# Performance work log

Hardware: AMD Instinct MI355X
Metric: run time of the kernel (lower is better)

## Reference

```python
import jax, jax.numpy as jnp
import numpy as np

D = 2048      # d_model
H = 16        # n_heads
DH = D // H   # head dim = 128
L = 512       # kv_latent_dim
B = 2
S = 2048      # new tokens
PAST = 2048   # cached latent positions


def _w(key, shape, fan_in):
    return jax.random.normal(key, shape, jnp.float32) * (fan_in ** -0.5)


def setup_inputs() -> dict:
    key = jax.random.key(0)
    ks = jax.random.split(key, 8)
    return {
        "x": jax.random.normal(ks[0], (B, S, D), jnp.float32),
        "kv_cache": jax.random.normal(ks[1], (B, PAST, L), jnp.float32),
        "W_q": _w(ks[2], (D, D), D),       # nn.Linear weight [out, in]
        "W_dkv": _w(ks[3], (L, D), D),
        "W_uk": _w(ks[4], (D, L), L),
        "W_uv": _w(ks[5], (D, L), L),
        "W_o": _w(ks[6], (D, D), D),
        "ln_g": jnp.ones((L,), jnp.float32),
        "ln_b": jnp.zeros((L,), jnp.float32),
        "past_length": PAST,
    }


def _layernorm(x, g, b, eps=1e-5):
    mu = jnp.mean(x, axis=-1, keepdims=True)
    var = jnp.mean((x - mu) ** 2, axis=-1, keepdims=True)
    return (x - mu) * jax.lax.rsqrt(var + eps) * g + b


def reference(x, kv_cache, W_q, W_dkv, W_uk, W_uv, W_o, ln_g, ln_b, past_length):
    Bx, Sx, _ = x.shape
    # absorbed_k = W_q.weight @ W_uk.weight -> [D, L] -> [H, dh, L]
    absorbed = (W_q @ W_uk).reshape(H, DH, L)
    # compress to latent KV and layernorm
    new_c = _layernorm(x @ W_dkv.T, ln_g, ln_b)          # [B, S, L]
    c_kv = jnp.concatenate([kv_cache, new_c], axis=1)    # [B, T, L]
    T = c_kv.shape[1]
    # decompress V only
    v = (c_kv @ W_uv.T).reshape(Bx, T, H, DH).transpose(0, 2, 1, 3)  # [B, H, T, dh]
    # absorbed Q/K: scores_h = x_h @ absorbed_k[h] @ c_kv^T
    q = x.reshape(Bx, Sx, H, DH)                          # [B, S, H, dh]
    tmp = jnp.einsum('bshd,hdl->bhsl', q, absorbed)       # [B, H, S, L]
    scale = jnp.float32(1.0 / np.sqrt(DH))
    scores = jnp.einsum('bhsl,btl->bhst', tmp, c_kv) * scale  # [B, H, S, T]
    # causal mask: row i attends to cols j with j <= i + past_length
    mask = jnp.tril(jnp.ones((Sx, T), dtype=bool), k=past_length)
    scores = jnp.where(mask, scores, -jnp.inf)
    w = jax.nn.softmax(scores, axis=-1)
    ctx = jnp.einsum('bhst,bhtd->bshd', w, v).reshape(Bx, Sx, D)
    out = ctx @ W_o.T
    return out, c_kv
```

## Files before the change

### kernel.cpp

```cpp
#include <hip/hip_runtime.h>
#include <cstdint>

#define DV 2048
#define HH 16
#define DHD 128
#define LL 512
#define BB 2

typedef __attribute__((ext_vector_type(8))) short bf16x8;
typedef __attribute__((ext_vector_type(4))) float f32x4;
typedef __attribute__((ext_vector_type(4))) int i32x4;

typedef __attribute__((address_space(1))) const void* gas_cp;
typedef __attribute__((address_space(3))) void* las_p;

__device__ __forceinline__ void gll16(const void* g, void* l) {
    __builtin_amdgcn_global_load_lds((gas_cp)g, (las_p)l, 16, 0, 0);
}

__device__ __forceinline__ unsigned short f2b(float f) {
    union { float f; unsigned int u; } v; v.f = f;
    unsigned int u = v.u;
    return (unsigned short)((u + 0x7FFFu + ((u >> 16) & 1u)) >> 16);
}

__device__ __forceinline__ unsigned int cvt_pk_bf16(float lo, float hi) {
    unsigned int r;
    asm("v_cvt_pk_bf16_f32 %0, %1, %2" : "=v"(r) : "v"(lo), "v"(hi));
    return r;
}

#if __has_builtin(__builtin_amdgcn_exp2f)
#define EX2(x) __builtin_amdgcn_exp2f(x)
#else
#define EX2(x) exp2f(x)
#endif

__global__ void cvt_k(const float* __restrict__ in, ushort* __restrict__ out, long n) {
    long stride = (long)gridDim.x * blockDim.x * 4;
    for (long i = ((long)blockIdx.x * blockDim.x + threadIdx.x) * 4; i < n; i += stride) {
        float4 f = *(const float4*)(in + i);
        *(ushort4*)(out + i) = make_ushort4(f2b(f.x), f2b(f.y), f2b(f.z), f2b(f.w));
    }
}

__global__ void transpose_cvt_k(const float* __restrict__ in, ushort* __restrict__ outp,
                                int R, int C) {
    __shared__ float tile[64][65];
    int c0 = blockIdx.x * 64, r0 = blockIdx.y * 64;
    int tx = threadIdx.x & 63, ty = threadIdx.x >> 6;
#pragma unroll
    for (int p = 0; p < 16; ++p)
        tile[ty + p * 4][tx] = in[(long)(r0 + ty + p * 4) * C + c0 + tx];
    __syncthreads();
#pragma unroll
    for (int p = 0; p < 16; ++p)
        outp[(long)(c0 + ty + p * 4) * R + r0 + tx] = f2b(tile[tx][ty + p * 4]);
}

__global__ void kvcopy_k(const float* __restrict__ kv, float* __restrict__ cko,
                         ushort* __restrict__ ckb, int PAST, int T) {
    long n = (long)BB * PAST * LL;
    long pl2 = (long)PAST * LL;
    long stride = (long)gridDim.x * blockDim.x * 4;
    for (long i = ((long)blockIdx.x * blockDim.x + threadIdx.x) * 4; i < n; i += stride) {
        float4 f = *(const float4*)(kv + i);
        long b = i / pl2, wloc = i - b * pl2;
        long o = b * (long)T * LL + wloc;
        *(float4*)(cko + o) = f;
        *(ushort4*)(ckb + o) = make_ushort4(f2b(f.x), f2b(f.y), f2b(f.z), f2b(f.w));
    }
}

__global__ __launch_bounds__(256) void ln_k(const float* __restrict__ cpre,
                                            const float* __restrict__ g, const float* __restrict__ be,
                                            float* __restrict__ cko, ushort* __restrict__ ckb,
                                            int S, int PAST, int T) {
    int wid = threadIdx.x >> 6, lane = threadIdx.x & 63;
    int row = blockIdx.x * 4 + wid;
    int b = row / S, s = row - b * S;
    const float* xr = cpre + (long)row * LL + lane * 8;
    float4 v0 = *(const float4*)xr;
    float4 v1 = *(const float4*)(xr + 4);
    float sum = v0.x + v0.y + v0.z + v0.w + v1.x + v1.y + v1.z + v1.w;
    float sq = v0.x * v0.x + v0.y * v0.y + v0.z * v0.z + v0.w * v0.w +
               v1.x * v1.x + v1.y * v1.y + v1.z * v1.z + v1.w * v1.w;
#pragma unroll
    for (int m = 1; m < 64; m <<= 1) { sum += __shfl_xor(sum, m, 64); sq += __shfl_xor(sq, m, 64); }
    float mu = sum * (1.0f / LL);
    float var = sq * (1.0f / LL) - mu * mu;
    float rstd = rsqrtf(var + 1e-5f);
    const float* gp = g + lane * 8;
    const float* bp = be + lane * 8;
    float4 g0 = *(const float4*)gp, g1 = *(const float4*)(gp + 4);
    float4 b0 = *(const float4*)bp, b1 = *(const float4*)(bp + 4);
    float y0 = (v0.x - mu) * rstd * g0.x + b0.x;
    float y1 = (v0.y - mu) * rstd * g0.y + b0.y;
    float y2 = (v0.z - mu) * rstd * g0.z + b0.z;
    float y3 = (v0.w - mu) * rstd * g0.w + b0.w;
    float y4 = (v1.x - mu) * rstd * g1.x + b1.x;
    float y5 = (v1.y - mu) * rstd * g1.y + b1.y;
    float y6 = (v1.z - mu) * rstd * g1.z + b1.z;
    float y7 = (v1.w - mu) * rstd * g1.w + b1.w;
    long o = ((long)b * T + PAST + s) * LL + lane * 8;
    *(float4*)(cko + o) = make_float4(y0, y1, y2, y3);
    *(float4*)(cko + o + 4) = make_float4(y4, y5, y6, y7);
    *(ushort4*)(ckb + o) = make_ushort4(f2b(y0), f2b(y1), f2b(y2), f2b(y3));
    *(ushort4*)(ckb + o + 4) = make_ushort4(f2b(y4), f2b(y5), f2b(y6), f2b(y7));
}

template <bool OUT_BF16>
__global__ __launch_bounds__(256, 2) void gemm_nt(const ushort* __restrict__ A,
                                                  const ushort* __restrict__ B,
                                                  void* __restrict__ Cv,
                                                  int K, int lda, int ldb, int ldc,
                                                  long aHi, long aLo, long bHi, long bLo,
                                                  long cHi, long cLo, int zdiv, float cscale) {
    __shared__ __align__(16) ushort Asm[128 * 72];
    __shared__ __align__(16) ushort Bsm[128 * 72];
    const int tid = threadIdx.x, wid = tid >> 6, lane = tid & 63;
    const int z = blockIdx.z, zh = z / zdiv, zl = z % zdiv;
    A += zh * aHi + zl * aLo;
    B += zh * bHi + zl * bLo;
    const long cOff = zh * cHi + zl * cLo;
    const int m0 = blockIdx.x * 128, n0 = blockIdx.y * 128;
    const int wm = (wid >> 1) * 64, wn = (wid & 1) * 64;
    f32x4 acc[4][4] = {};
    const int l8 = lane & 7;
    const int rowA = wid * 8 + (lane >> 3);
    const ushort* Ag = A + (long)(m0 + rowA) * lda + l8 * 8;
    const ushort* Bg = B + (long)(n0 + rowA) * ldb + l8 * 8;

    i32x4 ra[4], rb[4];
#pragma unroll
    for (int p = 0; p < 4; ++p) {
        ra[p] = *(const i32x4*)(Ag + (long)p * 32 * lda);
        rb[p] = *(const i32x4*)(Bg + (long)p * 32 * ldb);
    }
    for (int kt = 0; kt < K; kt += 64) {
        __syncthreads();
#pragma unroll
        for (int p = 0; p < 4; ++p) {
            *(i32x4*)(Asm + (p * 32 + rowA) * 72 + l8 * 8) = ra[p];
            *(i32x4*)(Bsm + (p * 32 + rowA) * 72 + l8 * 8) = rb[p];
        }
        __syncthreads();
        if (kt + 64 < K) {
#pragma unroll
            for (int p = 0; p < 4; ++p) {
                ra[p] = *(const i32x4*)(Ag + (long)p * 32 * lda + kt + 64);
                rb[p] = *(const i32x4*)(Bg + (long)p * 32 * ldb + kt + 64);
            }
        }
#pragma unroll
        for (int kk = 0; kk < 2; ++kk) {
            const int ko = kk * 32 + ((lane >> 4) << 3);
            bf16x8 af[4], bf[4];
#pragma unroll
            for (int i = 0; i < 4; ++i)
                af[i] = *(const bf16x8*)(Asm + (wm + i * 16 + (lane & 15)) * 72 + ko);
#pragma unroll
            for (int j = 0; j < 4; ++j)
                bf[j] = *(const bf16x8*)(Bsm + (wn + j * 16 + (lane & 15)) * 72 + ko);
#pragma unroll
            for (int i = 0; i < 4; ++i)
#pragma unroll
                for (int j = 0; j < 4; ++j)
                    acc[i][j] = __builtin_amdgcn_mfma_f32_16x16x32_bf16(af[i], bf[j], acc[i][j], 0, 0, 0);
        }
        __syncthreads();
    }
    const int cr = (lane >> 4) * 4, cc = lane & 15;
#pragma unroll
    for (int i = 0; i < 4; ++i) {
#pragma unroll
        for (int r = 0; r < 4; ++r) {
            const long row = m0 + wm + i * 16 + cr + r;
#pragma unroll
            for (int j = 0; j < 4; ++j) {
                const long col = n0 + wn + j * 16 + cc;
                if (OUT_BF16)
                    ((ushort*)Cv)[cOff + row * ldc + col] = f2b(acc[i][j][r] * cscale);
                else
                    ((float*)Cv)[cOff + row * ldc + col] = acc[i][j][r] * cscale;
            }
        }
    }
}

#define PH_WAIT4()                                               \
    do {                                                         \
        asm volatile("s_waitcnt vmcnt(4) lgkmcnt(0)" ::: "memory"); \
        __builtin_amdgcn_s_barrier();                            \
    } while (0)
#define PH_WAIT0()                                               \
    do {                                                         \
        asm volatile("s_waitcnt vmcnt(0) lgkmcnt(0)" ::: "memory"); \
        __builtin_amdgcn_s_barrier();                            \
    } while (0)
#define RD_BAR()                                                 \
    do {                                                         \
        asm volatile("s_waitcnt lgkmcnt(0)" ::: "memory");       \
        __builtin_amdgcn_s_barrier();                            \
    } while (0)

__global__ __launch_bounds__(256, 4) void attn_k(const ushort* __restrict__ qbf,
                                                 const ushort* __restrict__ ktb,
                                                 const ushort* __restrict__ vtb,
                                                 ushort* __restrict__ ctxb,
                                                 int S, int T, int PAST) {
    __shared__ __align__(16) ushort bufK[64 * 128];
    __shared__ __align__(16) ushort bufV[128 * 64];
    __shared__ __align__(16) ushort pl[4][16][64];
    const int tid = threadIdx.x, wid = tid >> 6, lane = tid & 63;
    const int nsb = S >> 6;
    const int nwg = BB * HH * nsb;
    const int cpx = nwg >> 3;
    const int id = (int)blockIdx.x;
    const int xcd = id & 7, k = id >> 3;
    const int r4 = k >> 5, c32 = k & 31;
    const int local = r4 * 32 + ((c32 + r4 * 8) & 31);
    const int orig = xcd * cpx + local;
    const int sblk = orig % nsb;
    const int h = (orig / nsb) % HH;
    const int b = orig / (nsb * HH);
    const int s0 = (nsb - 1 - sblk) * 64;

    const int g = lane >> 4, l15 = lane & 15, q8 = g << 3;
    const int swr = (l15 & 7) << 3;

    bf16x8 qf[4];
    {
        const ushort* qb = qbf + ((long)b * S + s0 + wid * 16 + l15) * DV + h * DHD + q8;
#pragma unroll
        for (int kk = 0; kk < 4; ++kk) qf[kk] = *(const bf16x8*)(qb + kk * 32);
    }
    f32x4 cacc[8] = {};
    f32x4 sacc[4] = {};
    float mrow = -1e30f, lrow = 0.f;
    const int rl = tid >> 4, cc16 = tid & 15;
    const int vr = tid >> 3, vc = tid & 7;
    const int nfull = (s0 + PAST) / 64;
    const ushort* kbase = ktb + (long)b * T * DV + h * DHD;
    const ushort* vbase = vtb + ((long)b * DV + h * DHD) * T;
    const int kcol = (cc16 ^ (rl & 7)) << 3;
    const int vcol = (vc ^ (vr & 7)) << 3;

    auto stageK = [&](int tt_) {
#pragma unroll
        for (int p = 0; p < 4; ++p)
            gll16(kbase + (long)(tt_ * 64 + p * 16 + rl) * DV + kcol, &bufK[p * 2048 + tid * 8]);
    };
    auto stageV = [&](int tt_) {
#pragma unroll
        for (int p = 0; p < 4; ++p)
            gll16(vbase + (long)(p * 32 + vr) * T + tt_ * 64 + vcol, &bufV[p * 2048 + tid * 8]);
    };

    stageK(0);
    stageV(0);

    for (int tt = 0; tt <= nfull; ++tt) {
        const bool last = (tt == nfull);
        PH_WAIT4();
        __builtin_amdgcn_s_setprio(1);
#pragma unroll
        for (int kk = 0; kk < 4; ++kk) {
            const int ko = kk * 32 + q8;
#pragma unroll
            for (int nf = 0; nf < 4; ++nf) {
                bf16x8 af = *(const bf16x8*)(&bufK[(nf * 16 + l15) * 128 + (ko ^ swr)]);
                sacc[nf] = __builtin_amdgcn_mfma_f32_16x16x32_bf16(af, qf[kk], sacc[nf], 0, 0, 0);
            }
        }
        __builtin_amdgcn_s_setprio(0);
        RD_BAR();
        if (!last) stageK(tt + 1);
        if (last) { PH_WAIT0(); } else { PH_WAIT4(); }
        float pm = -1e30f;
#pragma unroll
        for (int nf = 0; nf < 4; ++nf)
#pragma unroll
            for (int r = 0; r < 4; ++r) {
                float v = sacc[nf][r];
                if (last) {
                    int tl = nf * 16 + (g << 2) + r;
                    int ql = wid * 16 + l15;
                    if (tl > ql) v = -1e30f;
                }
                sacc[nf][r] = v;
                pm = fmaxf(pm, v);
            }
        pm = fmaxf(pm, __shfl_xor(pm, 16, 64));
        pm = fmaxf(pm, __shfl_xor(pm, 32, 64));
        if (__any(pm > mrow + 11.5f)) {
            float mn = fmaxf(mrow, pm);
            float al = EX2(mrow - mn);
            mrow = mn;
            lrow *= al;
#pragma unroll
            for (int r = 0; r < 4; ++r) {
                float alr = __shfl(al, (g << 2) + r, 64);
#pragma unroll
                for (int df = 0; df < 8; ++df) cacc[df][r] *= alr;
            }
        }
        float ps = 0.f;
#pragma unroll
        for (int nf = 0; nf < 4; ++nf)
#pragma unroll
            for (int r = 0; r < 4; ++r) {
                float p = EX2(sacc[nf][r] - mrow);
                sacc[nf][r] = p;
                ps += p;
            }
        ps += __shfl_xor(ps, 16, 64);
        ps += __shfl_xor(ps, 32, 64);
        lrow += ps;
#pragma unroll
        for (int nf = 0; nf < 4; ++nf)
#pragma unroll
            for (int rp = 0; rp < 2; ++rp) {
                unsigned int hb = cvt_pk_bf16(sacc[nf][rp * 2], sacc[nf][rp * 2 + 1]);
                const int tlo = nf * 16 + (g << 2) + rp * 2;
                *(unsigned int*)&pl[wid][l15][tlo ^ swr] = hb;
            }
#pragma unroll
        for (int nf = 0; nf < 4; ++nf) sacc[nf] = (f32x4){0.f, 0.f, 0.f, 0.f};
        __builtin_amdgcn_s_setprio(1);
#pragma unroll
        for (int kk = 0; kk < 2; ++kk) {
            bf16x8 a = *(const bf16x8*)(&pl[wid][l15][(kk * 32 + q8) ^ swr]);
#pragma unroll
            for (int df = 0; df < 8; ++df) {
                bf16x8 bv = *(const bf16x8*)(&bufV[(df * 16 + l15) * 64 + ((kk * 32 + q8) ^ swr)]);
                cacc[df] = __builtin_amdgcn_mfma_f32_16x16x32_bf16(a, bv, cacc[df], 0, 0, 0);
            }
        }
        __builtin_amdgcn_s_setprio(0);
        if (!last) {
            RD_BAR();
            stageV(tt + 1);
        }
    }
    const long rbase = (long)b * S + s0 + wid * 16 + (g << 2);
#pragma unroll
    for (int r = 0; r < 4; ++r) {
        float lr = __shfl(lrow, (g << 2) + r, 64);
        float inv = 1.0f / lr;
        const int d = h * DHD + l15;
#pragma unroll
        for (int df = 0; df < 8; ++df)
            ctxb[(rbase + r) * DV + d + df * 16] = f2b(cacc[df][r] * inv);
    }
}

extern "C" void kernel_launch(void* const* d_in, const int* in_sizes, int n_in,
                              void* d_out, int out_size, void* d_ws, size_t ws_size,
                              hipStream_t stream) {
    const float* x = (const float*)d_in[0];
    const float* kv = (const float*)d_in[1];
    const float* Wq = (const float*)d_in[2];
    const float* Wdkv = (const float*)d_in[3];
    const float* Wuk = (const float*)d_in[4];
    const float* Wuv = (const float*)d_in[5];
    const float* Wo = (const float*)d_in[6];
    const float* lng = (const float*)d_in[7];
    const float* lnbt = (const float*)d_in[8];
    const int S = in_sizes[0] / (BB * DV);
    const int PAST = in_sizes[1] / (BB * LL);
    const int T = S + PAST;

    float* out_p = (float*)d_out;
    float* ckv_out = out_p + (size_t)BB * S * DV;

    char* w = (char*)d_ws;
    auto take = [&](size_t bytes) { char* p = w; w += (bytes + 255) & ~(size_t)255; return p; };
    ushort* xb    = (ushort*)take((size_t)BB * S * DV * 2);
    ushort* Wqb   = (ushort*)take((size_t)DV * DV * 2);
    ushort* WukT  = (ushort*)take((size_t)DV * LL * 2);
    ushort* Wdkvb = (ushort*)take((size_t)LL * DV * 2);
    ushort* Wuvb  = (ushort*)take((size_t)DV * LL * 2);
    ushort* Wob   = (ushort*)take((size_t)DV * DV * 2);
    ushort* absb  = (ushort*)take((size_t)DV * LL * 2);
    float*  cpre  = (float*)take((size_t)BB * S * LL * 4);
    ushort* ckvb  = (ushort*)take((size_t)BB * T * LL * 2);
    ushort* vtb   = (ushort*)take((size_t)BB * DV * T * 2);
    ushort* ktb   = (ushort*)take((size_t)BB * T * DV * 2);
    ushort* ctxb  = (ushort*)take((size_t)BB * S * DV * 2);

    auto cvt = [&](const float* in, ushort* op, long n) {
        long nb = (n / 4 + 255) / 256;
        if (nb > 2048) nb = 2048;
        cvt_k<<<dim3((unsigned)nb), dim3(256), 0, stream>>>(in, op, n);
    };
    cvt(x, xb, (long)BB * S * DV);
    cvt(Wq, Wqb, (long)DV * DV);
    cvt(Wdkv, Wdkvb, (long)LL * DV);
    cvt(Wuv, Wuvb, (long)DV * LL);
    cvt(Wo, Wob, (long)DV * DV);
    transpose_cvt_k<<<dim3(LL / 64, DV / 64), dim3(256), 0, stream>>>(Wuk, WukT, DV, LL);
    kvcopy_k<<<dim3(2048), dim3(256), 0, stream>>>(kv, ckv_out, ckvb, PAST, T);

    gemm_nt<true><<<dim3(DV / 128, LL / 128, 1), dim3(256), 0, stream>>>(
        Wqb, WukT, absb, DV, DV, DV, LL, 0, 0, 0, 0, 0, 0, 1, 0.12751744900014818f);
    gemm_nt<false><<<dim3(BB * S / 128, LL / 128, 1), dim3(256), 0, stream>>>(
        xb, Wdkvb, cpre, DV, DV, DV, LL, 0, 0, 0, 0, 0, 0, 1, 1.0f);
    ln_k<<<dim3(BB * S / 4), dim3(256), 0, stream>>>(cpre, lng, lnbt, ckv_out, ckvb, S, PAST, T);
    gemm_nt<true><<<dim3(DV / 128, T / 128, BB), dim3(256), 0, stream>>>(
        Wuvb, ckvb, vtb, LL, LL, LL, T, 0, 0, (long)T * LL, 0, (long)DV * T, 0, 1, 1.0f);
    gemm_nt<true><<<dim3(T / 128, DV / 128, BB), dim3(256), 0, stream>>>(
        ckvb, absb, ktb, LL, LL, LL, DV, (long)T * LL, 0, 0, 0, (long)T * DV, 0, 1, 1.0f);
    attn_k<<<dim3(BB * HH * (S / 64)), dim3(256), 0, stream>>>(xb, ktb, vtb, ctxb, S, T, PAST);
    gemm_nt<false><<<dim3(BB * S / 128, DV / 128, 1), dim3(256), 0, stream>>>(
        ctxb, Wob, out_p, DV, DV, DV, DV, 0, 0, 0, 0, 0, 0, 1, 1.0f);
}
```

Before: 350.1 us.

## Use async global-to-LDS loads with double-buffered XOR-swizzled tiles in GEMM

```diff
diff --git a/kernel.cpp b/kernel.cpp
--- a/kernel.cpp
+++ b/kernel.cpp
@@ -109,15 +109,21 @@
     *(ushort4*)(ckb + o + 4) = make_ushort4(f2b(y4), f2b(y5), f2b(y6), f2b(y7));
 }
 
+#define G_WAIT()                                                    \
+    do {                                                            \
+        asm volatile("s_waitcnt vmcnt(0) lgkmcnt(0)" ::: "memory"); \
+        __builtin_amdgcn_s_barrier();                               \
+    } while (0)
+
 template <bool OUT_BF16>
-__global__ __launch_bounds__(256, 2) void gemm_nt(const ushort* __restrict__ A,
-                                                  const ushort* __restrict__ B,
-                                                  void* __restrict__ Cv,
-                                                  int K, int lda, int ldb, int ldc,
-                                                  long aHi, long aLo, long bHi, long bLo,
-                                                  long cHi, long cLo, int zdiv, float cscale) {
-    __shared__ __align__(16) ushort Asm[128 * 72];
-    __shared__ __align__(16) ushort Bsm[128 * 72];
+__global__ __launch_bounds__(256) void gemm_nt(const ushort* __restrict__ A,
+                                               const ushort* __restrict__ B,
+                                               void* __restrict__ Cv,
+                                               int K, int lda, int ldb, int ldc,
+                                               long aHi, long aLo, long bHi, long bLo,
+                                               long cHi, long cLo, int zdiv, float cscale) {
+    __shared__ __align__(16) ushort Asm[2][8192];
+    __shared__ __align__(16) ushort Bsm[2][8192];
     const int tid = threadIdx.x, wid = tid >> 6, lane = tid & 63;
     const int z = blockIdx.z, zh = z / zdiv, zl = z % zdiv;
     A += zh * aHi + zl * aLo;
@@ -125,52 +131,55 @@
     const long cOff = zh * cHi + zl * cLo;
     const int m0 = blockIdx.x * 128, n0 = blockIdx.y * 128;
     const int wm = (wid >> 1) * 64, wn = (wid & 1) * 64;
+    const int l15 = lane & 15;
+    const int swr = (l15 & 7) << 3;
+    const int vr = tid >> 3, vc = tid & 7;
+    const int scol = (vc ^ (vr & 7)) << 3;
     f32x4 acc[4][4] = {};
-    const int l8 = lane & 7;
-    const int rowA = wid * 8 + (lane >> 3);
-    const ushort* Ag = A + (long)(m0 + rowA) * lda + l8 * 8;
-    const ushort* Bg = B + (long)(n0 + rowA) * ldb + l8 * 8;
-
-    i32x4 ra[4], rb[4];
-#pragma unroll
-    for (int p = 0; p < 4; ++p) {
-        ra[p] = *(const i32x4*)(Ag + (long)p * 32 * lda);
-        rb[p] = *(const i32x4*)(Bg + (long)p * 32 * ldb);
-    }
-    for (int kt = 0; kt < K; kt += 64) {
-        __syncthreads();
-#pragma unroll
-        for (int p = 0; p < 4; ++p) {
-            *(i32x4*)(Asm + (p * 32 + rowA) * 72 + l8 * 8) = ra[p];
-            *(i32x4*)(Bsm + (p * 32 + rowA) * 72 + l8 * 8) = rb[p];
-        }
-        __syncthreads();
-        if (kt + 64 < K) {
-#pragma unroll
-            for (int p = 0; p < 4; ++p) {
-                ra[p] = *(const i32x4*)(Ag + (long)p * 32 * lda + kt + 64);
-                rb[p] = *(const i32x4*)(Bg + (long)p * 32 * ldb + kt + 64);
-            }
-        }
+
+    auto stageA = [&](int kt_, int bi) {
+#pragma unroll
+        for (int p = 0; p < 4; ++p)
+            gll16(A + (long)(m0 + p * 32 + vr) * lda + kt_ + scol,
+                  &Asm[bi][p * 2048 + tid * 8]);
+    };
+    auto stageB = [&](int kt_, int bi) {
+#pragma unroll
+        for (int p = 0; p < 4; ++p)
+            gll16(B + (long)(n0 + p * 32 + vr) * ldb + kt_ + scol,
+                  &Bsm[bi][p * 2048 + tid * 8]);
+    };
+
+    stageA(0, 0);
+    stageB(0, 0);
+    const int nkt = K >> 6;
+    for (int ki = 0; ki < nkt; ++ki) {
+        const int cur = ki & 1;
+        G_WAIT();
+        if (ki + 1 < nkt) {
+            stageA((ki + 1) << 6, cur ^ 1);
+            stageB((ki + 1) << 6, cur ^ 1);
+        }
+        __builtin_amdgcn_s_setprio(1);
 #pragma unroll
         for (int kk = 0; kk < 2; ++kk) {
             const int ko = kk * 32 + ((lane >> 4) << 3);
             bf16x8 af[4], bf[4];
 #pragma unroll
             for (int i = 0; i < 4; ++i)
-                af[i] = *(const bf16x8*)(Asm + (wm + i * 16 + (lane & 15)) * 72 + ko);
+                af[i] = *(const bf16x8*)(&Asm[cur][(wm + i * 16 + l15) * 64 + (ko ^ swr)]);
 #pragma unroll
             for (int j = 0; j < 4; ++j)
-                bf[j] = *(const bf16x8*)(Bsm + (wn + j * 16 + (lane & 15)) * 72 + ko);
+                bf[j] = *(const bf16x8*)(&Bsm[cur][(wn + j * 16 + l15) * 64 + (ko ^ swr)]);
 #pragma unroll
             for (int i = 0; i < 4; ++i)
 #pragma unroll
                 for (int j = 0; j < 4; ++j)
                     acc[i][j] = __builtin_amdgcn_mfma_f32_16x16x32_bf16(af[i], bf[j], acc[i][j], 0, 0, 0);
         }
-        __syncthreads();
-    }
-    const int cr = (lane >> 4) * 4, cc = lane & 15;
+        __builtin_amdgcn_s_setprio(0);
+    }
+    const int cr = (lane >> 4) * 4, cc = l15;
 #pragma unroll
     for (int i = 0; i < 4; ++i) {
 #pragma unroll
```

After: 357.5 us. 1.02x slower.
